# Performance work log

Measured on AMD Instinct MI355X. Metric: run time of the kernel, lower is better.

The kernel has to match this reference:

```python
import jax, jax.numpy as jnp
import numpy as np

O, C_IN, P, D = 256, 256, 96, 2
KH, KW = 51, 51


def setup_inputs() -> dict:
    key = jax.random.key(0)
    k1, k2, k3 = jax.random.split(key, 3)
    # coordinate grid in [-1, 1], shape (1, D, KH, KW) like a normalized meshgrid
    ys = jnp.linspace(-1.0, 1.0, KH, dtype=jnp.float32)
    xs = jnp.linspace(-1.0, 1.0, KW, dtype=jnp.float32)
    gy, gx = jnp.meshgrid(ys, xs, indexing="ij")
    x = jnp.stack([gy, gx], axis=0)[None]  # (1, 2, KH, KW)
    # learned point coordinates, trunc-normal-ish in [-1, 1]
    weight_coord = jnp.clip(0.3 * jax.random.normal(k1, (O, P, D), dtype=jnp.float32), -1.0, 1.0)
    # per-point radius, initialized to init_radius
    radius = jnp.full((O, P, 1, 1), 0.5, dtype=jnp.float32)
    # point weights
    weights = 0.02 * jax.random.normal(k2, (O, C_IN, P), dtype=jnp.float32)
    return {"x": x, "weight_coord": weight_coord, "radius": radius, "weights": weights}


def reference(x, weight_coord, radius, weights):
    o, p, d = weight_coord.shape
    spatial = x.shape[2:]  # (KH, KW)
    n = int(np.prod(spatial))
    coords = x.reshape(d, n).T  # (N, D)
    # broadcast coord diff + L1 distance over dim_linear: (O, P, N)
    dist = jnp.sum(jnp.abs(weight_coord[:, :, None, :] - coords[None, None, :, :]), axis=-1)
    # triangular basis
    vals = jax.nn.relu(1.0 - dist / radius.reshape(o, p, 1))  # (O, P, N)
    # count of points covering each location, used to normalize
    count = jnp.sum(vals != 0, axis=1, keepdims=True)  # (O, 1, N), int
    weighted = vals / (count.astype(vals.dtype) + 1e-6)
    # batched small matmul over points: (O, C_in, P) @ (O, P, N) -> (O, C_in, N)
    kernels = jnp.einsum("ocp,opn->ocn", weights, weighted)
    kernels = kernels.reshape(o, weights.shape[1], *spatial)
    # dim_linear == 2 branch: transpose last two dims, flip along dim 2
    kernels = jnp.flip(jnp.swapaxes(kernels, -2, -1), axis=2)
    return kernels
```

## Files before the change

kernel.cpp:

```cpp
#include <hip/hip_runtime.h>

#define O_DIM 256
#define C_DIM 256
#define P_DIM 96
#define KHW 51
#define NSP 2601
#define NST 41
#define CSPLIT 4
#define CB 64
#define PITCH 68

typedef __attribute__((ext_vector_type(8))) short short8v;
typedef __attribute__((ext_vector_type(4))) float float4v;
typedef __attribute__((ext_vector_type(4), aligned(16))) float float4a;
typedef __attribute__((ext_vector_type(4), aligned(4))) float float4u;

static __device__ __forceinline__ unsigned f2bf(float f) {
  union { float f; unsigned u; } v; v.f = f;
  return (v.u + 0x7FFFu + ((v.u >> 16) & 1u)) >> 16;
}
static __device__ __forceinline__ unsigned cvtpk(float lo, float hi) {
  unsigned r;
  asm("v_cvt_pk_bf16_f32 %0, %1, %2" : "=v"(r) : "v"(lo), "v"(hi));
  return r;
}

__global__ __launch_bounds__(256, 4) void smp_fused(
    const float* __restrict__ xg,
    const float* __restrict__ wc,
    const float* __restrict__ rad,
    const float* __restrict__ wts,
    float* __restrict__ out)
{
  __shared__ float Ylds[56];
  __shared__ float pyL[96], pxL[96], prL[96];
  __shared__ __align__(16) float Sl[2][64 * PITCH];

  const int b = blockIdx.x;
  const int o = b >> 2;
  const int cq = b & 3;
  const int tid = threadIdx.x;
  const int wave = tid >> 6;
  const int lane = tid & 63;
  const int row16 = lane & 15;
  const int kgrp = lane >> 4;

  if (tid < 51) Ylds[tid] = xg[tid * KHW];
  if (tid < 96) {
    pyL[tid] = wc[((size_t)o * P_DIM + tid) * 2];
    pxL[tid] = wc[((size_t)o * P_DIM + tid) * 2 + 1];
    prL[tid] = 1.0f / rad[(size_t)o * P_DIM + tid];
  }

  short8v wfr[4][3];
  {
    const float* Wo = wts + ((size_t)o * C_DIM + cq * CB) * P_DIM;
#pragma unroll
    for (int mf = 0; mf < 4; ++mf) {
      const float* src = Wo + (mf * 16 + row16) * P_DIM;
#pragma unroll
      for (int ks = 0; ks < 3; ++ks) {
        const float4 a4 = *(const float4*)(src + ks * 32 + kgrp * 8);
        const float4 c4 = *(const float4*)(src + ks * 32 + kgrp * 8 + 4);
        short8v f;
        f[0] = (short)f2bf(a4.x); f[1] = (short)f2bf(a4.y);
        f[2] = (short)f2bf(a4.z); f[3] = (short)f2bf(a4.w);
        f[4] = (short)f2bf(c4.x); f[5] = (short)f2bf(c4.y);
        f[6] = (short)f2bf(c4.z); f[7] = (short)f2bf(c4.w);
        wfr[mf][ks] = f;
      }
    }
  }
  __syncthreads();

  const int jb = wave * 16 + row16;
  const int q = tid & 15;
  const int h = tid >> 4;
  const size_t obase = ((size_t)o * C_DIM + cq * CB) * NSP;

  for (int st = 0; st < NST; ++st) {
    const int jl = st * 64 + jb;
    const int jc = jl < NSP ? jl : NSP - 1;
    const int i = jc / KHW;
    const int jj = jc - i * KHW;
    const float gy = Ylds[jj];
    const float gx = Ylds[50 - i];

    float4v acc[4];
#pragma unroll
    for (int mf = 0; mf < 4; ++mf) acc[mf] = (float4v){0.f, 0.f, 0.f, 0.f};

    int cnt = 0;
#pragma unroll
    for (int ks = 0; ks < 3; ++ks) {
      const int pb = ks * 32 + kgrp * 8;
      const float4a py0 = *(const float4a*)&pyL[pb];
      const float4a py1 = *(const float4a*)&pyL[pb + 4];
      const float4a px0 = *(const float4a*)&pxL[pb];
      const float4a px1 = *(const float4a*)&pxL[pb + 4];
      const float4a pr0 = *(const float4a*)&prL[pb];
      const float4a pr1 = *(const float4a*)&prL[pb + 4];
      float s[8], v[8];
#pragma unroll
      for (int j = 0; j < 4; ++j) {
        s[j]     = fmaf(fabsf(py0[j] - gy) + fabsf(px0[j] - gx), -pr0[j], 1.0f);
        s[j + 4] = fmaf(fabsf(py1[j] - gy) + fabsf(px1[j] - gx), -pr1[j], 1.0f);
      }
#pragma unroll
      for (int j = 0; j < 8; ++j) {
        v[j] = s[j] > 0.0f ? s[j] : 0.0f;
        cnt += (s[j] > 0.0f);
      }
      union { unsigned u[4]; short8v sv; } bfr;
#pragma unroll
      for (int jp = 0; jp < 4; ++jp) bfr.u[jp] = cvtpk(v[2 * jp], v[2 * jp + 1]);
#pragma unroll
      for (int mf = 0; mf < 4; ++mf)
        acc[mf] = __builtin_amdgcn_mfma_f32_16x16x32_bf16(
            wfr[mf][ks], bfr.sv, acc[mf], 0, 0, 0);
    }
    cnt += __shfl_xor(cnt, 16);
    cnt += __shfl_xor(cnt, 32);
    const float inv = __builtin_amdgcn_rcpf((float)cnt + 1e-6f);

    float* sl = &Sl[st & 1][0];
#pragma unroll
    for (int mf = 0; mf < 4; ++mf)
#pragma unroll
      for (int r = 0; r < 4; ++r)
        sl[(mf * 16 + kgrp * 4 + r) * PITCH + jb] = acc[mf][r] * inv;

    __syncthreads();

    if (st < NST - 1) {
#pragma unroll
      for (int i2 = 0; i2 < 4; ++i2) {
        const int row = h * 4 + i2;
        const float4a vv = *(const float4a*)&sl[row * PITCH + q * 4];
        float4u sv = {vv[0], vv[1], vv[2], vv[3]};
        *(float4u*)(out + obase + (size_t)row * NSP + st * 64 + q * 4) = sv;
      }
    } else {
      const int rem = NSP - (NST - 1) * 64;
#pragma unroll
      for (int i2 = 0; i2 < 4; ++i2) {
        const int row = h * 4 + i2;
        const float4a vv = *(const float4a*)&sl[row * PITCH + q * 4];
        float* gp = out + obase + (size_t)row * NSP + st * 64 + q * 4;
        if (q * 4 + 3 < rem) {
          float4u sv = {vv[0], vv[1], vv[2], vv[3]};
          *(float4u*)gp = sv;
        } else if (q * 4 < rem) {
#pragma unroll
          for (int r2 = 0; r2 < 4; ++r2)
            if (q * 4 + r2 < rem) gp[r2] = vv[r2];
        }
      }
    }
  }
}

extern "C" void kernel_launch(void* const* d_in, const int* in_sizes, int n_in,
                              void* d_out, int out_size, void* d_ws, size_t ws_size,
                              hipStream_t stream) {
  const float* xg  = (const float*)d_in[0];
  const float* wcp = (const float*)d_in[1];
  const float* rad = (const float*)d_in[2];
  const float* wts = (const float*)d_in[3];
  float* out = (float*)d_out;
  hipLaunchKernelGGL(smp_fused, dim3(O_DIM * CSPLIT), dim3(256), 0, stream,
                     xg, wcp, rad, wts, out);
}
```

Baseline: 234.5 us.

## Give each wave its own channel slice and drop block-wide barriers

The work split inside a block changes. Each wave now owns 16 output channels across all 64 spatial columns of a tile, instead of 16 columns across all 64 channels. Results are staged through a private per-wave LDS buffer, so the per-tile __syncthreads goes away and each wave keeps only one set of weight fragments in registers. The trade-off is that every wave recomputes the triangular basis and counts for all 64 columns, which quadruples that VALU work per block. The LDS pitch also changes.

```diff
diff --git a/kernel.cpp b/kernel.cpp
--- a/kernel.cpp
+++ b/kernel.cpp
@@ -6,9 +6,7 @@
 #define KHW 51
 #define NSP 2601
 #define NST 41
-#define CSPLIT 4
-#define CB 64
-#define PITCH 68
+#define PITCH 72
 
 typedef __attribute__((ext_vector_type(8))) short short8v;
 typedef __attribute__((ext_vector_type(4))) float float4v;
@@ -32,13 +30,13 @@
     const float* __restrict__ wts,
     float* __restrict__ out)
 {
-  __shared__ float Ylds[56];
-  __shared__ float pyL[96], pxL[96], prL[96];
-  __shared__ __align__(16) float Sl[2][64 * PITCH];
+  __shared__ float Ylds[52];
+  __shared__ __align__(16) float pyL[96], pxL[96], prL[96];
+  __shared__ __align__(16) float Sl[4][16 * PITCH];
 
   const int b = blockIdx.x;
   const int o = b >> 2;
-  const int cq = b & 3;
+  const int cqb = (b & 3) * 64;
   const int tid = threadIdx.x;
   const int wave = tid >> 6;
   const int lane = tid & 63;
@@ -52,45 +50,45 @@
     prL[tid] = 1.0f / rad[(size_t)o * P_DIM + tid];
   }
 
-  short8v wfr[4][3];
+  short8v wfr[3];
   {
-    const float* Wo = wts + ((size_t)o * C_DIM + cq * CB) * P_DIM;
+    const float* src = wts + ((size_t)o * C_DIM + cqb + wave * 16 + row16) * P_DIM;
 #pragma unroll
-    for (int mf = 0; mf < 4; ++mf) {
-      const float* src = Wo + (mf * 16 + row16) * P_DIM;
-#pragma unroll
-      for (int ks = 0; ks < 3; ++ks) {
-        const float4 a4 = *(const float4*)(src + ks * 32 + kgrp * 8);
-        const float4 c4 = *(const float4*)(src + ks * 32 + kgrp * 8 + 4);
-        short8v f;
-        f[0] = (short)f2bf(a4.x); f[1] = (short)f2bf(a4.y);
-        f[2] = (short)f2bf(a4.z); f[3] = (short)f2bf(a4.w);
-        f[4] = (short)f2bf(c4.x); f[5] = (short)f2bf(c4.y);
-        f[6] = (short)f2bf(c4.z); f[7] = (short)f2bf(c4.w);
-        wfr[mf][ks] = f;
-      }
+    for (int ks = 0; ks < 3; ++ks) {
+      const float4 a4 = *(const float4*)(src + ks * 32 + kgrp * 8);
+      const float4 c4 = *(const float4*)(src + ks * 32 + kgrp * 8 + 4);
+      short8v f;
+      f[0] = (short)f2bf(a4.x); f[1] = (short)f2bf(a4.y);
+      f[2] = (short)f2bf(a4.z); f[3] = (short)f2bf(a4.w);
+      f[4] = (short)f2bf(c4.x); f[5] = (short)f2bf(c4.y);
+      f[6] = (short)f2bf(c4.z); f[7] = (short)f2bf(c4.w);
+      wfr[ks] = f;
     }
   }
   __syncthreads();
 
-  const int jb = wave * 16 + row16;
-  const int q = tid & 15;
-  const int h = tid >> 4;
-  const size_t obase = ((size_t)o * C_DIM + cq * CB) * NSP;
+  float* sl = &Sl[wave][0];
+  const int jq = (lane & 15) * 4;
+  const int rq = lane >> 4;
+  const size_t obase = ((size_t)o * C_DIM + cqb + wave * 16) * NSP;
 
   for (int st = 0; st < NST; ++st) {
-    const int jl = st * 64 + jb;
-    const int jc = jl < NSP ? jl : NSP - 1;
-    const int i = jc / KHW;
-    const int jj = jc - i * KHW;
-    const float gy = Ylds[jj];
-    const float gx = Ylds[50 - i];
+    float gys[4], gxs[4];
+#pragma unroll
+    for (int jf = 0; jf < 4; ++jf) {
+      int jl = st * 64 + jf * 16 + row16;
+      int jc = jl < NSP ? jl : NSP - 1;
+      int i = jc / KHW;
+      int jj = jc - i * KHW;
+      gys[jf] = Ylds[jj];
+      gxs[jf] = Ylds[50 - i];
+    }
 
     float4v acc[4];
 #pragma unroll
-    for (int mf = 0; mf < 4; ++mf) acc[mf] = (float4v){0.f, 0.f, 0.f, 0.f};
+    for (int jf = 0; jf < 4; ++jf) acc[jf] = (float4v){0.f, 0.f, 0.f, 0.f};
+    int cnt[4] = {0, 0, 0, 0};
 
-    int cnt = 0;
 #pragma unroll
     for (int ks = 0; ks < 3; ++ks) {
       const int pb = ks * 32 + kgrp * 8;
@@ -100,60 +98,60 @@
       const float4a px1 = *(const float4a*)&pxL[pb + 4];
       const float4a pr0 = *(const float4a*)&prL[pb];
       const float4a pr1 = *(const float4a*)&prL[pb + 4];
-      float s[8], v[8];
 #pragma unroll
-      for (int j = 0; j < 4; ++j) {
-        s[j]     = fmaf(fabsf(py0[j] - gy) + fabsf(px0[j] - gx), -pr0[j], 1.0f);
-        s[j + 4] = fmaf(fabsf(py1[j] - gy) + fabsf(px1[j] - gx), -pr1[j], 1.0f);
+      for (int jf = 0; jf < 4; ++jf) {
+        const float gy = gys[jf], gx = gxs[jf];
+        float s[8], v[8];
+#pragma unroll
+        for (int j = 0; j < 4; ++j) {
+          s[j]     = fmaf(fabsf(py0[j] - gy) + fabsf(px0[j] - gx), -pr0[j], 1.0f);
+          s[j + 4] = fmaf(fabsf(py1[j] - gy) + fabsf(px1[j] - gx), -pr1[j], 1.0f);
+        }
+#pragma unroll
+        for (int j = 0; j < 8; ++j) {
+          v[j] = s[j] > 0.0f ? s[j] : 0.0f;
+          cnt[jf] += (s[j] > 0.0f);
+        }
+        union { unsigned u[4]; short8v sv; } bfr;
+#pragma unroll
+        for (int jp = 0; jp < 4; ++jp) bfr.u[jp] = cvtpk(v[2 * jp], v[2 * jp + 1]);
+        acc[jf] = __builtin_amdgcn_mfma_f32_16x16x32_bf16(
+            wfr[ks], bfr.sv, acc[jf], 0, 0, 0);
       }
+    }
+
 #pragma unroll
-      for (int j = 0; j < 8; ++j) {
-        v[j] = s[j] > 0.0f ? s[j] : 0.0f;
-        cnt += (s[j] > 0.0f);
-      }
-      union { unsigned u[4]; short8v sv; } bfr;
-#pragma unroll
-      for (int jp = 0; jp < 4; ++jp) bfr.u[jp] = cvtpk(v[2 * jp], v[2 * jp + 1]);
-#pragma unroll
-      for (int mf = 0; mf < 4; ++mf)
-        acc[mf] = __builtin_amdgcn_mfma_f32_16x16x32_bf16(
-            wfr[mf][ks], bfr.sv, acc[mf], 0, 0, 0);
-    }
-    cnt += __shfl_xor(cnt, 16);
-    cnt += __shfl_xor(cnt, 32);
-    const float inv = __builtin_amdgcn_rcpf((float)cnt + 1e-6f);
-
-    float* sl = &Sl[st & 1][0];
-#pragma unroll
-    for (int mf = 0; mf < 4; ++mf)
+    for (int jf = 0; jf < 4; ++jf) {
+      cnt[jf] += __shfl_xor(cnt[jf], 16);
+      cnt[jf] += __shfl_xor(cnt[jf], 32);
+      const float inv = __builtin_amdgcn_rcpf((float)cnt[jf] + 1e-6f);
 #pragma unroll
       for (int r = 0; r < 4; ++r)
-        sl[(mf * 16 + kgrp * 4 + r) * PITCH + jb] = acc[mf][r] * inv;
-
-    __syncthreads();
+        sl[(kgrp * 4 + r) * PITCH + jf * 16 + row16] = acc[jf][r] * inv;
+    }
 
     if (st < NST - 1) {
 #pragma unroll
       for (int i2 = 0; i2 < 4; ++i2) {
-        const int row = h * 4 + i2;
-        const float4a vv = *(const float4a*)&sl[row * PITCH + q * 4];
+        const int row = i2 * 4 + rq;
+        const float4a vv = *(const float4a*)&sl[row * PITCH + jq];
         float4u sv = {vv[0], vv[1], vv[2], vv[3]};
-        *(float4u*)(out + obase + (size_t)row * NSP + st * 64 + q * 4) = sv;
+        *(float4u*)(out + obase + (size_t)row * NSP + st * 64 + jq) = sv;
       }
     } else {
       const int rem = NSP - (NST - 1) * 64;
 #pragma unroll
       for (int i2 = 0; i2 < 4; ++i2) {
-        const int row = h * 4 + i2;
-        const float4a vv = *(const float4a*)&sl[row * PITCH + q * 4];
-        float* gp = out + obase + (size_t)row * NSP + st * 64 + q * 4;
-        if (q * 4 + 3 < rem) {
+        const int row = i2 * 4 + rq;
+        const float4a vv = *(const float4a*)&sl[row * PITCH + jq];
+        float* gp = out + obase + (size_t)row * NSP + st * 64 + jq;
+        if (jq + 3 < rem) {
           float4u sv = {vv[0], vv[1], vv[2], vv[3]};
           *(float4u*)gp = sv;
-        } else if (q * 4 < rem) {
+        } else if (jq < rem) {
 #pragma unroll
           for (int r2 = 0; r2 < 4; ++r2)
-            if (q * 4 + r2 < rem) gp[r2] = vv[r2];
+            if (jq + r2 < rem) gp[r2] = vv[r2];
         }
       }
     }
@@ -168,6 +166,6 @@
   const float* rad = (const float*)d_in[2];
   const float* wts = (const float*)d_in[3];
   float* out = (float*)d_out;
-  hipLaunchKernelGGL(smp_fused, dim3(O_DIM * CSPLIT), dim3(256), 0, stream,
+  hipLaunchKernelGGL(smp_fused, dim3(O_DIM * 4), dim3(256), 0, stream,
                      xg, wcp, rad, wts, out);
 }
```

Result: slower. 254.4 us (+8.5%).

## Split spatial dimension across blocks and stage a full 512-column tile in LDS

Applied to the files above, without the earlier changes.

The grid now also splits the 2601 spatial positions into 6 chunks of 512, so there are six times as many blocks, each with 512 threads. Each block computes its whole 64x512 output tile into one large LDS buffer, syncs once, then writes rows as long contiguous runs. This replaces the per-64-column double-buffered loop, which synced on every step, and is meant to raise parallelism and make stores more coalesced. In exchange, every block reloads the weight fragments and point parameters. The roughly 136 KB LDS buffer likely limits the CU to one block, and compute no longer overlaps with stores inside a block.

```diff
diff --git a/kernel.cpp b/kernel.cpp
--- a/kernel.cpp
+++ b/kernel.cpp
@@ -5,10 +5,9 @@
 #define P_DIM 96
 #define KHW 51
 #define NSP 2601
-#define NST 41
-#define CSPLIT 4
-#define CB 64
-#define PITCH 68
+#define JPH 512
+#define NJS 6
+#define PITCH 532
 
 typedef __attribute__((ext_vector_type(8))) short short8v;
 typedef __attribute__((ext_vector_type(4))) float float4v;
@@ -25,20 +24,22 @@
   return r;
 }
 
-__global__ __launch_bounds__(256, 4) void smp_fused(
+__global__ __launch_bounds__(512, 2) void smp_fused(
     const float* __restrict__ xg,
     const float* __restrict__ wc,
     const float* __restrict__ rad,
     const float* __restrict__ wts,
     float* __restrict__ out)
 {
-  __shared__ float Ylds[56];
-  __shared__ float pyL[96], pxL[96], prL[96];
-  __shared__ __align__(16) float Sl[2][64 * PITCH];
+  __shared__ float Ylds[52];
+  __shared__ __align__(16) float pyL[96], pxL[96], prL[96];
+  __shared__ __align__(16) float RB[64 * PITCH];
 
   const int b = blockIdx.x;
-  const int o = b >> 2;
-  const int cq = b & 3;
+  const int js = b % NJS;
+  const int cq = (b / NJS) & 3;
+  const int o = b / (NJS * 4);
+  const int jl0 = js * JPH;
   const int tid = threadIdx.x;
   const int wave = tid >> 6;
   const int lane = tid & 63;
@@ -54,7 +55,7 @@
 
   short8v wfr[4][3];
   {
-    const float* Wo = wts + ((size_t)o * C_DIM + cq * CB) * P_DIM;
+    const float* Wo = wts + ((size_t)o * C_DIM + cq * 64) * P_DIM;
 #pragma unroll
     for (int mf = 0; mf < 4; ++mf) {
       const float* src = Wo + (mf * 16 + row16) * P_DIM;
@@ -73,13 +74,10 @@
   }
   __syncthreads();
 
-  const int jb = wave * 16 + row16;
-  const int q = tid & 15;
-  const int h = tid >> 4;
-  const size_t obase = ((size_t)o * C_DIM + cq * CB) * NSP;
-
-  for (int st = 0; st < NST; ++st) {
-    const int jl = st * 64 + jb;
+  const int nsteps = (js == NJS - 1) ? 1 : 4;
+  for (int step = 0; step < nsteps; ++step) {
+    const int jlc = step * 128 + wave * 16 + row16;
+    const int jl = jl0 + jlc;
     const int jc = jl < NSP ? jl : NSP - 1;
     const int i = jc / KHW;
     const int jj = jc - i * KHW;
@@ -89,8 +87,8 @@
     float4v acc[4];
 #pragma unroll
     for (int mf = 0; mf < 4; ++mf) acc[mf] = (float4v){0.f, 0.f, 0.f, 0.f};
+    int cnt = 0;
 
-    int cnt = 0;
 #pragma unroll
     for (int ks = 0; ks < 3; ++ks) {
       const int pb = ks * 32 + kgrp * 8;
@@ -123,38 +121,43 @@
     cnt += __shfl_xor(cnt, 32);
     const float inv = __builtin_amdgcn_rcpf((float)cnt + 1e-6f);
 
-    float* sl = &Sl[st & 1][0];
 #pragma unroll
     for (int mf = 0; mf < 4; ++mf)
 #pragma unroll
       for (int r = 0; r < 4; ++r)
-        sl[(mf * 16 + kgrp * 4 + r) * PITCH + jb] = acc[mf][r] * inv;
+        RB[(mf * 16 + kgrp * 4 + r) * PITCH + jlc] = acc[mf][r] * inv;
+  }
+  __syncthreads();
 
-    __syncthreads();
-
-    if (st < NST - 1) {
+  const size_t obase = ((size_t)o * C_DIM + cq * 64) * NSP;
+  if (js < NJS - 1) {
 #pragma unroll
-      for (int i2 = 0; i2 < 4; ++i2) {
-        const int row = h * 4 + i2;
-        const float4a vv = *(const float4a*)&sl[row * PITCH + q * 4];
-        float4u sv = {vv[0], vv[1], vv[2], vv[3]};
-        *(float4u*)(out + obase + (size_t)row * NSP + st * 64 + q * 4) = sv;
+    for (int r2 = 0; r2 < 8; ++r2) {
+      const int row = wave * 8 + r2;
+      float* gp = out + obase + (size_t)row * NSP + jl0;
+#pragma unroll
+      for (int h2 = 0; h2 < 2; ++h2) {
+        const int col = h2 * 256 + lane * 4;
+        const float4a v = *(const float4a*)&RB[row * PITCH + col];
+        float4u sv = {v[0], v[1], v[2], v[3]};
+        *(float4u*)(gp + col) = sv;
       }
-    } else {
-      const int rem = NSP - (NST - 1) * 64;
+    }
+  } else {
+    const int rem = NSP - jl0;
 #pragma unroll
-      for (int i2 = 0; i2 < 4; ++i2) {
-        const int row = h * 4 + i2;
-        const float4a vv = *(const float4a*)&sl[row * PITCH + q * 4];
-        float* gp = out + obase + (size_t)row * NSP + st * 64 + q * 4;
-        if (q * 4 + 3 < rem) {
-          float4u sv = {vv[0], vv[1], vv[2], vv[3]};
-          *(float4u*)gp = sv;
-        } else if (q * 4 < rem) {
+    for (int r2 = 0; r2 < 8; ++r2) {
+      const int row = wave * 8 + r2;
+      const int col = lane * 4;
+      float* gp = out + obase + (size_t)row * NSP + jl0 + col;
+      const float4a v = *(const float4a*)&RB[row * PITCH + col];
+      if (col + 4 <= rem) {
+        float4u sv = {v[0], v[1], v[2], v[3]};
+        *(float4u*)gp = sv;
+      } else if (col < rem) {
 #pragma unroll
-          for (int r2 = 0; r2 < 4; ++r2)
-            if (q * 4 + r2 < rem) gp[r2] = vv[r2];
-        }
+        for (int r3 = 0; r3 < 4; ++r3)
+          if (col + r3 < rem) gp[r3] = v[r3];
       }
     }
   }
@@ -168,6 +171,6 @@
   const float* rad = (const float*)d_in[2];
   const float* wts = (const float*)d_in[3];
   float* out = (float*)d_out;
-  hipLaunchKernelGGL(smp_fused, dim3(O_DIM * CSPLIT), dim3(256), 0, stream,
+  hipLaunchKernelGGL(smp_fused, dim3(O_DIM * 4 * NJS), dim3(512), 0, stream,
                      xg, wcp, rad, wts, out);
 }
```

Result: slower. 297.8 us (+27.0%).

## Split into basis-precompute kernel and workspace-fed MFMA GEMM with bf16 LDS staging

Applied to the files above, without the earlier changes.

Replaces the single fused kernel with two kernels. The first computes the normalized triangular basis values once per output channel and stores them as bf16 in the workspace. The second runs a GEMM over 16-row channel groups that reads the basis from the workspace, stages results in LDS as bf16, and writes them out as float. This removes the 4x redundant basis computation across channel quarters, but adds a write and read of a large workspace buffer, lowers occupancy with a large LDS buffer, and rounds the output to bf16 precision. The old fused kernel is kept as a fallback when the workspace is too small.

```diff
diff --git a/kernel.cpp b/kernel.cpp
--- a/kernel.cpp
+++ b/kernel.cpp
@@ -5,15 +5,12 @@
 #define P_DIM 96
 #define KHW 51
 #define NSP 2601
-#define NST 41
-#define CSPLIT 4
-#define CB 64
-#define PITCH 68
+#define WS_NEED ((size_t)O_DIM * NSP * P_DIM * 2)
 
 typedef __attribute__((ext_vector_type(8))) short short8v;
 typedef __attribute__((ext_vector_type(4))) float float4v;
 typedef __attribute__((ext_vector_type(4), aligned(16))) float float4a;
-typedef __attribute__((ext_vector_type(4), aligned(4))) float float4u;
+typedef __attribute__((ext_vector_type(4), aligned(16))) unsigned uint4a;
 
 static __device__ __forceinline__ unsigned f2bf(float f) {
   union { float f; unsigned u; } v; v.f = f;
@@ -25,17 +22,132 @@
   return r;
 }
 
-__global__ __launch_bounds__(256, 4) void smp_fused(
-    const float* __restrict__ xg,
-    const float* __restrict__ wc,
-    const float* __restrict__ rad,
-    const float* __restrict__ wts,
-    float* __restrict__ out)
-{
+__global__ __launch_bounds__(256) void smp_vals(
+    const float* __restrict__ xg, const float* __restrict__ wc,
+    const float* __restrict__ rad, unsigned* __restrict__ ws32) {
+  const int b = blockIdx.x;
+  const int o = b / 41;
+  const int ch = b - o * 41;
+  const int tid = threadIdx.x;
+  const int jlloc = tid >> 2;
+  const int sp = tid & 3;
+  const int jl = ch * 64 + jlloc;
+  const int jc = jl < NSP ? jl : NSP - 1;
+  const int i = jc / KHW;
+  const int jj = jc - i * KHW;
+  const int n = jj * KHW + (KHW - 1 - i);
+  const float gy = xg[n];
+  const float gx = xg[NSP + n];
+  const float* wp = wc + ((size_t)o * P_DIM + sp * 24) * 2;
+  const float* rp = rad + (size_t)o * P_DIM + sp * 24;
+
+  float t[24];
+  int cnt = 0;
+#pragma unroll
+  for (int k = 0; k < 24; ++k) {
+    const float prk = 1.0f / rp[k];
+    float d = fabsf(wp[2 * k] - gy) + fabsf(wp[2 * k + 1] - gx);
+    float s = fmaf(d, -prk, 1.0f);
+    t[k] = s > 0.0f ? s : 0.0f;
+    cnt += (s > 0.0f);
+  }
+  cnt += __shfl_xor(cnt, 1);
+  cnt += __shfl_xor(cnt, 2);
+  const float inv = __builtin_amdgcn_rcpf((float)cnt + 1e-6f);
+
+  if (jl < NSP) {
+    unsigned u[12];
+#pragma unroll
+    for (int k = 0; k < 12; ++k) u[k] = cvtpk(t[2 * k] * inv, t[2 * k + 1] * inv);
+    unsigned* dst = ws32 + (size_t)o * (NSP * 48) + jl * 48 + sp * 12;
+#pragma unroll
+    for (int q = 0; q < 3; ++q) {
+      uint4a v = {u[q * 4], u[q * 4 + 1], u[q * 4 + 2], u[q * 4 + 3]};
+      *(uint4a*)(dst + q * 4) = v;
+    }
+  }
+}
+
+__global__ __launch_bounds__(1024, 1) void smp_gemm(
+    const unsigned short* __restrict__ ws, const float* __restrict__ wts,
+    float* __restrict__ out) {
+  __shared__ unsigned short RBuf[16 * NSP];
+
+  const int b = blockIdx.x;
+  const int swz = (b & 7) * 512 + (b >> 3);
+  const int o = swz >> 4;
+  const int cg = swz & 15;
+  const int tid = threadIdx.x;
+  const int wave = tid >> 6;
+  const int lane = tid & 63;
+  const int row16 = lane & 15;
+  const int kgrp = lane >> 4;
+
+  short8v wfr[3];
+  {
+    const float* src = wts + ((size_t)o * C_DIM + cg * 16 + row16) * P_DIM;
+#pragma unroll
+    for (int ks = 0; ks < 3; ++ks) {
+      const float4 a4 = *(const float4*)(src + ks * 32 + kgrp * 8);
+      const float4 c4 = *(const float4*)(src + ks * 32 + kgrp * 8 + 4);
+      short8v f;
+      f[0] = (short)f2bf(a4.x); f[1] = (short)f2bf(a4.y);
+      f[2] = (short)f2bf(a4.z); f[3] = (short)f2bf(a4.w);
+      f[4] = (short)f2bf(c4.x); f[5] = (short)f2bf(c4.y);
+      f[6] = (short)f2bf(c4.z); f[7] = (short)f2bf(c4.w);
+      wfr[ks] = f;
+    }
+  }
+
+  const unsigned short* wso = ws + (size_t)o * (NSP * P_DIM);
+
+  for (int r = 0; r < 11; ++r) {
+    const int jlb = r * 256 + wave * 16;
+    if (jlb < NSP) {
+      const int jl = jlb + row16;
+      const int jc = jl < NSP ? jl : NSP - 1;
+      float4v acc = (float4v){0.f, 0.f, 0.f, 0.f};
+#pragma unroll
+      for (int ks = 0; ks < 3; ++ks) {
+        const short8v bfr = *(const short8v*)(wso + (size_t)jc * P_DIM + ks * 32 + kgrp * 8);
+        acc = __builtin_amdgcn_mfma_f32_16x16x32_bf16(wfr[ks], bfr, acc, 0, 0, 0);
+      }
+      if (jl < NSP) {
+#pragma unroll
+        for (int r2 = 0; r2 < 4; ++r2)
+          RBuf[(kgrp * 4 + r2) * NSP + jl] = (unsigned short)f2bf(acc[r2]);
+      }
+    }
+  }
+  __syncthreads();
+
+  const size_t gbase = ((size_t)o * C_DIM + cg * 16) * NSP;
+#pragma unroll
+  for (int k = 0; k < 11; ++k) {
+    const int idx4 = tid + k * 1024;
+    if (idx4 < 10404) {
+      const uint2 u = *(const uint2*)&RBuf[idx4 * 4];
+      float4a v;
+      union { unsigned u; float f; } c0, c1, c2, c3;
+      c0.u = (u.x & 0xFFFF0000u);  c1.u = (u.x << 16);
+      c2.u = (u.y & 0xFFFF0000u);  c3.u = (u.y << 16);
+      v[0] = c1.f; v[1] = c0.f; v[2] = c3.f; v[3] = c2.f;
+      *(float4a*)(out + gbase + (size_t)idx4 * 4) = v;
+    }
+  }
+}
+
+#define NST 41
+#define PITCH 68
+typedef __attribute__((ext_vector_type(4), aligned(4))) float float4u;
+
+__global__ __launch_bounds__(256, 4) void smp_fb(
+    const float* __restrict__ xg, const float* __restrict__ wc,
+    const float* __restrict__ rad, const float* __restrict__ wts,
+    float* __restrict__ out) {
   __shared__ float Ylds[56];
   __shared__ float pyL[96], pxL[96], prL[96];
   __shared__ __align__(16) float Sl[2][64 * PITCH];
-
   const int b = blockIdx.x;
   const int o = b >> 2;
   const int cq = b & 3;
@@ -44,17 +156,15 @@
   const int lane = tid & 63;
   const int row16 = lane & 15;
   const int kgrp = lane >> 4;
-
   if (tid < 51) Ylds[tid] = xg[tid * KHW];
   if (tid < 96) {
     pyL[tid] = wc[((size_t)o * P_DIM + tid) * 2];
     pxL[tid] = wc[((size_t)o * P_DIM + tid) * 2 + 1];
     prL[tid] = 1.0f / rad[(size_t)o * P_DIM + tid];
   }
-
   short8v wfr[4][3];
   {
-    const float* Wo = wts + ((size_t)o * C_DIM + cq * CB) * P_DIM;
+    const float* Wo = wts + ((size_t)o * C_DIM + cq * 64) * P_DIM;
 #pragma unroll
     for (int mf = 0; mf < 4; ++mf) {
       const float* src = Wo + (mf * 16 + row16) * P_DIM;
@@ -72,12 +182,10 @@
     }
   }
   __syncthreads();
-
   const int jb = wave * 16 + row16;
   const int q = tid & 15;
   const int h = tid >> 4;
-  const size_t obase = ((size_t)o * C_DIM + cq * CB) * NSP;
-
+  const size_t obase = ((size_t)o * C_DIM + cq * 64) * NSP;
   for (int st = 0; st < NST; ++st) {
     const int jl = st * 64 + jb;
     const int jc = jl < NSP ? jl : NSP - 1;
@@ -85,11 +193,9 @@
     const int jj = jc - i * KHW;
     const float gy = Ylds[jj];
     const float gx = Ylds[50 - i];
-
     float4v acc[4];
 #pragma unroll
     for (int mf = 0; mf < 4; ++mf) acc[mf] = (float4v){0.f, 0.f, 0.f, 0.f};
-
     int cnt = 0;
 #pragma unroll
     for (int ks = 0; ks < 3; ++ks) {
@@ -116,22 +222,18 @@
       for (int jp = 0; jp < 4; ++jp) bfr.u[jp] = cvtpk(v[2 * jp], v[2 * jp + 1]);
 #pragma unroll
       for (int mf = 0; mf < 4; ++mf)
-        acc[mf] = __builtin_amdgcn_mfma_f32_16x16x32_bf16(
-            wfr[mf][ks], bfr.sv, acc[mf], 0, 0, 0);
+        acc[mf] = __builtin_amdgcn_mfma_f32_16x16x32_bf16(wfr[mf][ks], bfr.sv, acc[mf], 0, 0, 0);
     }
     cnt += __shfl_xor(cnt, 16);
     cnt += __shfl_xor(cnt, 32);
     const float inv = __builtin_amdgcn_rcpf((float)cnt + 1e-6f);
-
     float* sl = &Sl[st & 1][0];
 #pragma unroll
     for (int mf = 0; mf < 4; ++mf)
 #pragma unroll
       for (int r = 0; r < 4; ++r)
         sl[(mf * 16 + kgrp * 4 + r) * PITCH + jb] = acc[mf][r] * inv;
-
     __syncthreads();
-
     if (st < NST - 1) {
 #pragma unroll
       for (int i2 = 0; i2 < 4; ++i2) {
@@ -168,6 +270,13 @@
   const float* rad = (const float*)d_in[2];
   const float* wts = (const float*)d_in[3];
   float* out = (float*)d_out;
-  hipLaunchKernelGGL(smp_fused, dim3(O_DIM * CSPLIT), dim3(256), 0, stream,
-                     xg, wcp, rad, wts, out);
-}
+  if (ws_size >= WS_NEED) {
+    hipLaunchKernelGGL(smp_vals, dim3(O_DIM * 41), dim3(256), 0, stream,
+                       xg, wcp, rad, (unsigned*)d_ws);
+    hipLaunchKernelGGL(smp_gemm, dim3(4096), dim3(1024), 0, stream,
+                       (const unsigned short*)d_ws, wts, out);
+  } else {
+    hipLaunchKernelGGL(smp_fb, dim3(O_DIM * 4), dim3(256), 0, stream,
+                       xg, wcp, rad, wts, out);
+  }
+}
```

New measurement: 427.5 us. 82.3% more time.
